# Performance work log

Hardware: AMD Instinct MI355X
Metric: run time of the kernel (lower is better)

Reference implementation:

```python
import jax, jax.numpy as jnp
import numpy as np

K = 7          # kernel_size
G = 16         # group_number
C = 256        # channel
R = 4          # reduction_ratio
BN_EPS = 1e-3  # keras BatchNormalization default epsilon


def setup_inputs() -> dict:
    key = jax.random.key(0)
    ks = jax.random.split(key, 8)
    B, H, W = 2, 64, 64
    Cr = C // R
    x = jax.random.normal(ks[0], (B, H, W, C), dtype=jnp.float32)
    # kernel_gen params: 1x1 conv (C->C/r), BN, ReLU, 1x1 conv (C/r -> K*K*G)
    w1 = jax.random.normal(ks[1], (C, Cr), dtype=jnp.float32) * (1.0 / np.sqrt(C))
    b1 = jnp.zeros((Cr,), dtype=jnp.float32)
    gamma = jnp.ones((Cr,), dtype=jnp.float32) + 0.1 * jax.random.normal(ks[2], (Cr,), dtype=jnp.float32)
    beta = 0.1 * jax.random.normal(ks[3], (Cr,), dtype=jnp.float32)
    mu = 0.1 * jax.random.normal(ks[4], (Cr,), dtype=jnp.float32)
    var = jnp.ones((Cr,), dtype=jnp.float32) + 0.05 * jax.random.uniform(ks[5], (Cr,), dtype=jnp.float32)
    w2 = jax.random.normal(ks[6], (Cr, K * K * G), dtype=jnp.float32) * (1.0 / np.sqrt(Cr))
    b2 = jnp.zeros((K * K * G,), dtype=jnp.float32)
    return {"x": x, "w1": w1, "b1": b1, "gamma": gamma, "beta": beta,
            "mu": mu, "var": var, "w2": w2, "b2": b2}


def reference(x, w1, b1, gamma, beta, mu, var, w2, b2):
    B, H, W, _ = x.shape
    # stride == 1 -> stride_layer is identity; kernel_input = x
    # kernel_gen: 1x1 conv -> BN (inference) -> ReLU -> 1x1 conv
    t = jnp.einsum('bhwc,cd->bhwd', x, w1) + b1
    t = gamma * (t - mu) * jax.lax.rsqrt(var + BN_EPS) + beta
    t = jax.nn.relu(t)
    kern = jnp.einsum('bhwd,dk->bhwk', t, w2) + b2            # (B,H,W,K*K*G)
    kern = kern.reshape(B, H, W, K * K, 1, G)                  # (B,H,W,KK,1,G)
    # tf.image.extract_patches SAME, stride 1 -> pad K//2 each side, zeros
    pad = K // 2
    xp = jnp.pad(x, ((0, 0), (pad, pad), (pad, pad), (0, 0)))
    # patch layout matches TF: (kh, kw) outer, channel inner
    patches = jnp.stack(
        [xp[:, i:i + H, j:j + W, :] for i in range(K) for j in range(K)],
        axis=3)                                                # (B,H,W,KK,C)
    patches = patches.reshape(B, H, W, K * K, C // G, G)
    out = jnp.sum(kern * patches, axis=3)                      # (B,H,W,C/G,G)
    out = out.reshape(B, H, W, C)
    return out, kern
```

## Files before the change

kernel.cpp:

```cpp
#include <hip/hip_runtime.h>


typedef __attribute__((ext_vector_type(8))) short short8;
typedef __attribute__((ext_vector_type(4))) float f32x4;

#define OUT_ELEMS 2097152
#define W2S_OFF 0
#define W1S_OFF 131072
#define BNS_OFF (131072 + 32768)
#define BNH_OFF (BNS_OFF + 256)

static __device__ __forceinline__ ushort f2bf(float f) {
    union { float f; unsigned u; } v; v.f = f;
    return (ushort)((v.u + 0x7FFFu + ((v.u >> 16) & 1u)) >> 16);
}

__global__ __launch_bounds__(256)
void prep(const float* __restrict__ w1, const float* __restrict__ w2,
          const float* __restrict__ b1, const float* __restrict__ gamma_,
          const float* __restrict__ beta_, const float* __restrict__ mu_,
          const float* __restrict__ var_, char* __restrict__ base)
{
    const int g = blockIdx.x * 256 + threadIdx.x;
    ushort* w2s = (ushort*)(base + W2S_OFF);
    ushort* w1s = (ushort*)(base + W1S_OFF);
    float*  bns = (float*)(base + BNS_OFF);
    float*  bnh = (float*)(base + BNH_OFF);
    if (g < 50176) {
        const int e = g & 7, lane = (g >> 3) & 63, kgks = g >> 9;
        const int kg = kgks >> 1, ks = kgks & 1;
        const int n = kg * 16 + (lane & 15);
        const int k = ks * 32 + ((lane >> 4) << 3) + e;
        w2s[g] = f2bf(w2[k * 784 + n]);
    } else if (g < 66560) {
        const int e2 = g - 50176;
        const int e = e2 & 7, lane = (e2 >> 3) & 63, ntks = e2 >> 9;
        const int nt = ntks >> 3, ks = ntks & 7;
        const int n = nt * 16 + (lane & 15);
        const int k = ks * 32 + ((lane >> 4) << 3) + e;
        w1s[e2] = f2bf(w1[k * 64 + n]);
    } else if (g < 66624) {
        const int d = g - 66560;
        const float s = gamma_[d] * rsqrtf(var_[d] + 1e-3f);
        bns[d] = s;
        bnh[d] = beta_[d] + (b1[d] - mu_[d]) * s;
    }
}

__global__ __launch_bounds__(256)
void kern_gen(const float* __restrict__ x, const char* __restrict__ base,
              const float* __restrict__ b2, float* __restrict__ kern_out)
{
    __shared__ __align__(16) ushort xb[8192];
    __shared__ __align__(16) ushort tb[2048];

    const ushort* w2s = (const ushort*)(base + W2S_OFF);
    const ushort* w1s = (const ushort*)(base + W1S_OFF);
    const float*  bns = (const float*)(base + BNS_OFF);
    const float*  bnh = (const float*)(base + BNH_OFF);

    const int tid  = threadIdx.x;
    const int lane = tid & 63;
    const int wv   = tid >> 6;
    const int lin  = blockIdx.x;
    const int xcd  = lin & 7;
    const int rr_  = lin >> 3;
    const int tile = xcd * 32 + (rr_ & 31);
    const int khalf = rr_ >> 5;
    const int px0  = tile * 32;

#pragma unroll
    for (int i = 0; i < 8; ++i) {
        const int f4 = tid + 256 * i;
        const int px = f4 >> 6;
        const int c0 = (f4 & 63) * 4;
        const float4 v = *(const float4*)(x + (size_t)(px0 + px) * 256 + c0);
        ushort4 hh;
        hh.x = f2bf(v.x); hh.y = f2bf(v.y); hh.z = f2bf(v.z); hh.w = f2bf(v.w);
        const int byte = ((px << 9) + (c0 << 1)) ^ ((px & 7) << 4);
        *(ushort4*)((char*)xb + byte) = hh;
    }
    __syncthreads();

    const int qlane = lane >> 4;
    const int mrow  = lane & 15;
    const int rt    = wv & 1;
    const int nh    = wv >> 1;
    const int apx   = rt * 16 + mrow;
    const int aswz  = (apx & 7) << 4;

    f32x4 acc0 = {0.f, 0.f, 0.f, 0.f}, acc1 = {0.f, 0.f, 0.f, 0.f};
#pragma unroll
    for (int ks = 0; ks < 8; ++ks) {
        const short8 a = *(const short8*)((const char*)xb +
                          (((apx << 9) + ((ks * 32 + qlane * 8) << 1)) ^ aswz));
        const short8 bv0 = *(const short8*)(w1s + (((nh * 2 + 0) * 8 + ks) * 64 + lane) * 8);
        const short8 bv1 = *(const short8*)(w1s + (((nh * 2 + 1) * 8 + ks) * 64 + lane) * 8);
        acc0 = __builtin_amdgcn_mfma_f32_16x16x32_bf16(a, bv0, acc0, 0, 0, 0);
        acc1 = __builtin_amdgcn_mfma_f32_16x16x32_bf16(a, bv1, acc1, 0, 0, 0);
    }
#pragma unroll
    for (int half = 0; half < 2; ++half) {
        const f32x4 A = half ? acc1 : acc0;
        const int col = (nh * 2 + half) * 16 + mrow;
        const float s = bns[col], sh = bnh[col];
#pragma unroll
        for (int r = 0; r < 4; ++r) {
            const int row = rt * 16 + qlane * 4 + r;
            const float tv = fmaxf(fmaf(A[r], s, sh), 0.f);
            const int byte = ((row << 7) + (col << 1)) ^ ((row & 7) << 4);
            *(ushort*)((char*)tb + byte) = f2bf(tv);
        }
    }
    __syncthreads();

    const short8 a0 = *(const short8*)((const char*)tb +
                        (((apx << 7) + (qlane << 4)) ^ aswz));
    const short8 a1 = *(const short8*)((const char*)tb +
                        (((apx << 7) + 64 + (qlane << 4)) ^ aswz));
    const int kb = khalf ? 25 : 0;
    const int ke = khalf ? 49 : 25;
    for (int kg = kb + nh; kg < ke; kg += 2) {
        const short8 bv0 = *(const short8*)(w2s + (size_t)((kg * 2 + 0) * 64 + lane) * 8);
        const short8 bv1 = *(const short8*)(w2s + (size_t)((kg * 2 + 1) * 64 + lane) * 8);
        f32x4 c = {0.f, 0.f, 0.f, 0.f};
        c = __builtin_amdgcn_mfma_f32_16x16x32_bf16(a0, bv0, c, 0, 0, 0);
        c = __builtin_amdgcn_mfma_f32_16x16x32_bf16(a1, bv1, c, 0, 0, 0);
        const int n = kg * 16 + mrow;
        const float bias = b2[n];
#pragma unroll
        for (int r = 0; r < 4; ++r) {
            const int row = rt * 16 + qlane * 4 + r;
            kern_out[(size_t)(px0 + row) * 784 + n] = c[r] + bias;
        }
    }
}

#define FMA4(A, K, X) \
    A.x = fmaf(K.x, X.x, A.x); A.y = fmaf(K.y, X.y, A.y); \
    A.z = fmaf(K.z, X.z, A.z); A.w = fmaf(K.w, X.w, A.w);

__global__ __launch_bounds__(256)
void involution_apply(const float* __restrict__ x,
                      const float* __restrict__ kern,
                      float* __restrict__ out)
{
    __shared__ __align__(16) float kl[16 * 784];
    const int tid  = threadIdx.x;
    const int lane = tid & 63;
    const int wv   = tid >> 6;
    const int bid  = blockIdx.x;
    const int pb   = ((bid & 7) << 10) + ((bid >> 3) << 4);
    const int b  = pb >> 12;
    const int h  = (pb >> 6) & 63;
    const int w0 = pb & 63;

#pragma unroll
    for (int rr = 0; rr < 16; ++rr) {
        if (tid < 196)
            ((float4*)(kl + rr * 784))[tid] =
                ((const float4*)(kern + (size_t)(pb + rr) * 784))[tid];
    }
    __syncthreads();

    const int c0  = lane * 4;
    const int g0  = c0 & 15;
    const int w0w = w0 + wv * 4;
    const float* xbase = x + ((size_t)b << 20);

    float msk[10]; int colc[10];
#pragma unroll
    for (int j = 0; j < 10; ++j) {
        const int cw = w0w + j - 3;
        msk[j]  = ((unsigned)cw < 64u) ? 1.0f : 0.0f;
        colc[j] = (min(max(cw, 0), 63) << 8) + c0;
    }

    float4 acc[4];
#pragma unroll
    for (int p = 0; p < 4; ++p) acc[p] = make_float4(0.f, 0.f, 0.f, 0.f);

#pragma unroll
    for (int kh = 0; kh < 7; ++kh) {
        const int hh = h + kh - 3;
        if ((unsigned)hh < 64u) {
            const float* xr = xbase + ((size_t)hh << 14);
            float4 xv[10];
#pragma unroll
            for (int j = 0; j < 10; ++j) {
                xv[j] = *(const float4*)(xr + colc[j]);
                xv[j].x *= msk[j]; xv[j].y *= msk[j];
                xv[j].z *= msk[j]; xv[j].w *= msk[j];
            }
#pragma unroll
            for (int p = 0; p < 4; ++p) {
                const float* kr = kl + (wv * 4 + p) * 784 + kh * 112 + g0;
#pragma unroll
                for (int kw = 0; kw < 7; ++kw) {
                    const float4 kv = *(const float4*)(kr + kw * 16);
                    FMA4(acc[p], kv, xv[p + kw]);
                }
            }
        }
    }
#pragma unroll
    for (int p = 0; p < 4; ++p)
        *(float4*)(out + (size_t)(pb + wv * 4 + p) * 256 + c0) = acc[p];
}

extern "C" void kernel_launch(void* const* d_in, const int* in_sizes, int n_in,
                              void* d_out, int out_size, void* d_ws, size_t ws_size,
                              hipStream_t stream)
{
    const float* x      = (const float*)d_in[0];
    const float* w1     = (const float*)d_in[1];
    const float* b1     = (const float*)d_in[2];
    const float* gamma_ = (const float*)d_in[3];
    const float* beta_  = (const float*)d_in[4];
    const float* mu_    = (const float*)d_in[5];
    const float* var_   = (const float*)d_in[6];
    const float* w2     = (const float*)d_in[7];
    const float* b2     = (const float*)d_in[8];

    float* out  = (float*)d_out;
    float* kern = out + OUT_ELEMS;
    char*  base = (char*)d_out;

    prep<<<261, 256, 0, stream>>>(w1, w2, b1, gamma_, beta_, mu_, var_, base);
    kern_gen<<<512, 256, 0, stream>>>(x, base, b2, kern);
    involution_apply<<<512, 256, 0, stream>>>(x, kern, out);
}
```

Before: 109.0 us.

## Fuse kernel generation and involution apply into one kernel via shared memory

Merges the kernel-generation kernel and the involution-apply kernel into a single launch. Each block of 16 pixels computes its own generated kernel with MFMA, writes it to global output and directly into LDS. The apply stage then reads from LDS instead of re-reading the kernel tensor from global memory. This removes one launch and a global round trip, at the cost of less parallelism per block in the generation phase and an LDS union that limits reuse.

```diff
diff --git a/kernel.cpp b/kernel.cpp
--- a/kernel.cpp
+++ b/kernel.cpp
@@ -47,105 +47,25 @@
     }
 }
 
+#define FMA4(A, K, X) \
+    A.x = fmaf(K.x, X.x, A.x); A.y = fmaf(K.y, X.y, A.y); \
+    A.z = fmaf(K.z, X.z, A.z); A.w = fmaf(K.w, X.w, A.w);
+
 __global__ __launch_bounds__(256)
-void kern_gen(const float* __restrict__ x, const char* __restrict__ base,
-              const float* __restrict__ b2, float* __restrict__ kern_out)
+void invol_fused(const float* __restrict__ x, const char* __restrict__ base,
+                 const float* __restrict__ b2, float* __restrict__ kern_out,
+                 float* __restrict__ out)
 {
-    __shared__ __align__(16) ushort xb[8192];
-    __shared__ __align__(16) ushort tb[2048];
+    __shared__ __align__(16) union {
+        struct { ushort xb[4096]; ushort tb[1024]; } s;
+        float kl[12544];
+    } u;
 
     const ushort* w2s = (const ushort*)(base + W2S_OFF);
     const ushort* w1s = (const ushort*)(base + W1S_OFF);
     const float*  bns = (const float*)(base + BNS_OFF);
     const float*  bnh = (const float*)(base + BNH_OFF);
 
-    const int tid  = threadIdx.x;
-    const int lane = tid & 63;
-    const int wv   = tid >> 6;
-    const int lin  = blockIdx.x;
-    const int xcd  = lin & 7;
-    const int rr_  = lin >> 3;
-    const int tile = xcd * 32 + (rr_ & 31);
-    const int khalf = rr_ >> 5;
-    const int px0  = tile * 32;
-
-#pragma unroll
-    for (int i = 0; i < 8; ++i) {
-        const int f4 = tid + 256 * i;
-        const int px = f4 >> 6;
-        const int c0 = (f4 & 63) * 4;
-        const float4 v = *(const float4*)(x + (size_t)(px0 + px) * 256 + c0);
-        ushort4 hh;
-        hh.x = f2bf(v.x); hh.y = f2bf(v.y); hh.z = f2bf(v.z); hh.w = f2bf(v.w);
-        const int byte = ((px << 9) + (c0 << 1)) ^ ((px & 7) << 4);
-        *(ushort4*)((char*)xb + byte) = hh;
-    }
-    __syncthreads();
-
-    const int qlane = lane >> 4;
-    const int mrow  = lane & 15;
-    const int rt    = wv & 1;
-    const int nh    = wv >> 1;
-    const int apx   = rt * 16 + mrow;
-    const int aswz  = (apx & 7) << 4;
-
-    f32x4 acc0 = {0.f, 0.f, 0.f, 0.f}, acc1 = {0.f, 0.f, 0.f, 0.f};
-#pragma unroll
-    for (int ks = 0; ks < 8; ++ks) {
-        const short8 a = *(const short8*)((const char*)xb +
-                          (((apx << 9) + ((ks * 32 + qlane * 8) << 1)) ^ aswz));
-        const short8 bv0 = *(const short8*)(w1s + (((nh * 2 + 0) * 8 + ks) * 64 + lane) * 8);
-        const short8 bv1 = *(const short8*)(w1s + (((nh * 2 + 1) * 8 + ks) * 64 + lane) * 8);
-        acc0 = __builtin_amdgcn_mfma_f32_16x16x32_bf16(a, bv0, acc0, 0, 0, 0);
-        acc1 = __builtin_amdgcn_mfma_f32_16x16x32_bf16(a, bv1, acc1, 0, 0, 0);
-    }
-#pragma unroll
-    for (int half = 0; half < 2; ++half) {
-        const f32x4 A = half ? acc1 : acc0;
-        const int col = (nh * 2 + half) * 16 + mrow;
-        const float s = bns[col], sh = bnh[col];
-#pragma unroll
-        for (int r = 0; r < 4; ++r) {
-            const int row = rt * 16 + qlane * 4 + r;
-            const float tv = fmaxf(fmaf(A[r], s, sh), 0.f);
-            const int byte = ((row << 7) + (col << 1)) ^ ((row & 7) << 4);
-            *(ushort*)((char*)tb + byte) = f2bf(tv);
-        }
-    }
-    __syncthreads();
-
-    const short8 a0 = *(const short8*)((const char*)tb +
-                        (((apx << 7) + (qlane << 4)) ^ aswz));
-    const short8 a1 = *(const short8*)((const char*)tb +
-                        (((apx << 7) + 64 + (qlane << 4)) ^ aswz));
-    const int kb = khalf ? 25 : 0;
-    const int ke = khalf ? 49 : 25;
-    for (int kg = kb + nh; kg < ke; kg += 2) {
-        const short8 bv0 = *(const short8*)(w2s + (size_t)((kg * 2 + 0) * 64 + lane) * 8);
-        const short8 bv1 = *(const short8*)(w2s + (size_t)((kg * 2 + 1) * 64 + lane) * 8);
-        f32x4 c = {0.f, 0.f, 0.f, 0.f};
-        c = __builtin_amdgcn_mfma_f32_16x16x32_bf16(a0, bv0, c, 0, 0, 0);
-        c = __builtin_amdgcn_mfma_f32_16x16x32_bf16(a1, bv1, c, 0, 0, 0);
-        const int n = kg * 16 + mrow;
-        const float bias = b2[n];
-#pragma unroll
-        for (int r = 0; r < 4; ++r) {
-            const int row = rt * 16 + qlane * 4 + r;
-            kern_out[(size_t)(px0 + row) * 784 + n] = c[r] + bias;
-        }
-    }
-}
-
-#define FMA4(A, K, X) \
-    A.x = fmaf(K.x, X.x, A.x); A.y = fmaf(K.y, X.y, A.y); \
-    A.z = fmaf(K.z, X.z, A.z); A.w = fmaf(K.w, X.w, A.w);
-
-__global__ __launch_bounds__(256)
-void involution_apply(const float* __restrict__ x,
-                      const float* __restrict__ kern,
-                      float* __restrict__ out)
-{
-    __shared__ __align__(16) float kl[16 * 784];
     const int tid  = threadIdx.x;
     const int lane = tid & 63;
     const int wv   = tid >> 6;
@@ -156,10 +76,64 @@
     const int w0 = pb & 63;
 
 #pragma unroll
-    for (int rr = 0; rr < 16; ++rr) {
-        if (tid < 196)
-            ((float4*)(kl + rr * 784))[tid] =
-                ((const float4*)(kern + (size_t)(pb + rr) * 784))[tid];
+    for (int i = 0; i < 4; ++i) {
+        const int f4 = tid + 256 * i;
+        const int px = f4 >> 6;
+        const int c0 = (f4 & 63) * 4;
+        const float4 v = *(const float4*)(x + (size_t)(pb + px) * 256 + c0);
+        ushort4 hh;
+        hh.x = f2bf(v.x); hh.y = f2bf(v.y); hh.z = f2bf(v.z); hh.w = f2bf(v.w);
+        const int byte = ((px << 9) + (c0 << 1)) ^ ((px & 7) << 4);
+        *(ushort4*)((char*)u.s.xb + byte) = hh;
+    }
+    __syncthreads();
+
+    const int qlane = lane >> 4;
+    const int mrow  = lane & 15;
+    const int aswz  = (mrow & 7) << 4;
+
+    f32x4 acc = {0.f, 0.f, 0.f, 0.f};
+#pragma unroll
+    for (int ks = 0; ks < 8; ++ks) {
+        const short8 a = *(const short8*)((const char*)u.s.xb +
+                          (((mrow << 9) + ((ks * 32 + qlane * 8) << 1)) ^ aswz));
+        const short8 bv = *(const short8*)(w1s + ((wv * 8 + ks) * 64 + lane) * 8);
+        acc = __builtin_amdgcn_mfma_f32_16x16x32_bf16(a, bv, acc, 0, 0, 0);
+    }
+    {
+        const int col = wv * 16 + mrow;
+        const float s = bns[col], sh = bnh[col];
+#pragma unroll
+        for (int r = 0; r < 4; ++r) {
+            const int row = qlane * 4 + r;
+            const float tv = fmaxf(fmaf(acc[r], s, sh), 0.f);
+            const int byte = ((row << 7) + (col << 1)) ^ ((row & 7) << 4);
+            *(ushort*)((char*)u.s.tb + byte) = f2bf(tv);
+        }
+    }
+    __syncthreads();
+
+    const short8 a0 = *(const short8*)((const char*)u.s.tb +
+                        (((mrow << 7) + (qlane << 4)) ^ aswz));
+    const short8 a1 = *(const short8*)((const char*)u.s.tb +
+                        (((mrow << 7) + 64 + (qlane << 4)) ^ aswz));
+    __syncthreads();
+
+    for (int kg = wv; kg < 49; kg += 4) {
+        const short8 bv0 = *(const short8*)(w2s + (size_t)((kg * 2 + 0) * 64 + lane) * 8);
+        const short8 bv1 = *(const short8*)(w2s + (size_t)((kg * 2 + 1) * 64 + lane) * 8);
+        f32x4 c = {0.f, 0.f, 0.f, 0.f};
+        c = __builtin_amdgcn_mfma_f32_16x16x32_bf16(a0, bv0, c, 0, 0, 0);
+        c = __builtin_amdgcn_mfma_f32_16x16x32_bf16(a1, bv1, c, 0, 0, 0);
+        const int n = kg * 16 + mrow;
+        const float bias = b2[n];
+#pragma unroll
+        for (int r = 0; r < 4; ++r) {
+            const int row = qlane * 4 + r;
+            const float val = c[r] + bias;
+            kern_out[(size_t)(pb + row) * 784 + n] = val;
+            u.kl[row * 784 + n] = val;
+        }
     }
     __syncthreads();
 
@@ -176,9 +150,9 @@
         colc[j] = (min(max(cw, 0), 63) << 8) + c0;
     }
 
-    float4 acc[4];
-#pragma unroll
-    for (int p = 0; p < 4; ++p) acc[p] = make_float4(0.f, 0.f, 0.f, 0.f);
+    float4 acc4[4];
+#pragma unroll
+    for (int p = 0; p < 4; ++p) acc4[p] = make_float4(0.f, 0.f, 0.f, 0.f);
 
 #pragma unroll
     for (int kh = 0; kh < 7; ++kh) {
@@ -194,18 +168,18 @@
             }
 #pragma unroll
             for (int p = 0; p < 4; ++p) {
-                const float* kr = kl + (wv * 4 + p) * 784 + kh * 112 + g0;
+                const float* kr = u.kl + (wv * 4 + p) * 784 + kh * 112 + g0;
 #pragma unroll
                 for (int kw = 0; kw < 7; ++kw) {
                     const float4 kv = *(const float4*)(kr + kw * 16);
-                    FMA4(acc[p], kv, xv[p + kw]);
+                    FMA4(acc4[p], kv, xv[p + kw]);
                 }
             }
         }
     }
 #pragma unroll
     for (int p = 0; p < 4; ++p)
-        *(float4*)(out + (size_t)(pb + wv * 4 + p) * 256 + c0) = acc[p];
+        *(float4*)(out + (size_t)(pb + wv * 4 + p) * 256 + c0) = acc4[p];
 }
 
 extern "C" void kernel_launch(void* const* d_in, const int* in_sizes, int n_in,
@@ -227,6 +201,5 @@
     char*  base = (char*)d_out;
 
     prep<<<261, 256, 0, stream>>>(w1, w2, b1, gamma_, beta_, mu_, var_, base);
-    kern_gen<<<512, 256, 0, stream>>>(x, base, b2, kern);
-    involution_apply<<<512, 256, 0, stream>>>(x, kern, out);
-}
+    invol_fused<<<512, 256, 0, stream>>>(x, base, b2, kern, out);
+}
```

After: 96.23 us. 1.13x faster.
